# Kernel optimization log

Measured on AMD Instinct MI355X. Metric: run time of the kernel, lower is better.

The kernel has to match this reference:

```python
import jax, jax.numpy as jnp
import numpy as np
import math

B, T, P, E, H = 4, 64, 256, 512, 8
D = E // H
LN_EPS = 1e-5


def setup_inputs() -> dict:
    key = jax.random.key(0)
    ks = jax.random.split(key, 6)
    s = 0.02  # weight init scale
    return {
        "x": jax.random.normal(ks[0], (B, T, P, E), jnp.float32),
        "Wq": jax.random.normal(ks[1], (E, E), jnp.float32) * s,
        "bq": jnp.zeros((E,), jnp.float32),
        "Wk": jax.random.normal(ks[2], (E, E), jnp.float32) * s,
        "bk": jnp.zeros((E,), jnp.float32),
        "Wv": jax.random.normal(ks[3], (E, E), jnp.float32) * s,
        "bv": jnp.zeros((E,), jnp.float32),
        "Wo": jax.random.normal(ks[4], (E, E), jnp.float32) * s,
        "bo": jnp.zeros((E,), jnp.float32),
        "ln_g": jnp.ones((E,), jnp.float32),
        "ln_b": jnp.zeros((E,), jnp.float32),
    }


def _proj(x, W, b):
    # torch nn.Linear: y = x @ W.T + b
    return jnp.einsum('btpe,fe->btpf', x, W) + b


def _heads(y):
    # b t p (h d) -> b p h t d
    b, t, p, e = y.shape
    return y.reshape(b, t, p, H, D).transpose(0, 2, 3, 1, 4)


def reference(x, Wq, bq, Wk, bk, Wv, bv, Wo, bo, ln_g, ln_b):
    b, t, p, e = x.shape
    q = _heads(_proj(x, Wq, bq))  # [B,P,H,T,D]
    k = _heads(_proj(x, Wk, bk))
    v = _heads(_proj(x, Wv, bv))

    scores = jnp.einsum('bphtd,bphsd->bphts', q, k) / math.sqrt(D)
    causal_mask = jnp.triu(jnp.ones((t, t), dtype=bool), k=1)  # True above diag
    scores = jnp.where(causal_mask, -jnp.inf, scores)
    attn = jax.nn.softmax(scores, axis=-1)
    o = jnp.einsum('bphts,bphsd->bphtd', attn, v)

    # b p h t d -> b t p (h d)
    o = o.transpose(0, 3, 1, 2, 4).reshape(b, t, p, e)
    attn_out = jnp.einsum('btpe,fe->btpf', o, Wo) + bo

    y = x + attn_out
    # AdaptiveNormalizer with conditioning=None -> plain LayerNorm over E
    mu = jnp.mean(y, axis=-1, keepdims=True)
    var = jnp.var(y, axis=-1, keepdims=True)
    return (y - mu) * jax.lax.rsqrt(var + LN_EPS) * ln_g + ln_b
```

## Files before the change

### kernel.cpp

```cpp
#include <hip/hip_runtime.h>
#include <stdint.h>

#define B_ 4
#define T_ 64
#define P_ 256
#define E_ 512
#define H_ 8
#define D_ 64
#define NF 1536
#define MCH 16384

typedef unsigned short u16;
typedef __attribute__((ext_vector_type(8))) __bf16 bf16x8;
typedef __attribute__((ext_vector_type(4))) float f32x4;
typedef __attribute__((ext_vector_type(16))) float f32x16;

__device__ __forceinline__ u16 f2bf(float x) {
  union { float f; uint32_t u; } a; a.f = x;
  uint32_t u = a.u;
  uint32_t r = (u + 0x7FFFu + ((u >> 16) & 1u)) >> 16;
  return (u16)r;
}

__device__ __forceinline__ bf16x8 ld8(const u16* p) {
  union { uint4 u; bf16x8 b; } t;
  t.u = *reinterpret_cast<const uint4*>(p);
  return t.b;
}

typedef __attribute__((address_space(3))) void lds_void;
typedef __attribute__((address_space(1))) void g_void;
__device__ __forceinline__ void gl_lds16(const void* g, void* l) {
  __builtin_amdgcn_global_load_lds((g_void*)g, (lds_void*)l, 16, 0, 0);
}

__device__ __forceinline__ f32x4 mfma16(bf16x8 a, bf16x8 b, f32x4 c) {
  return __builtin_amdgcn_mfma_f32_16x16x32_bf16(a, b, c, 0, 0, 0);
}
__device__ __forceinline__ f32x16 mfma32(bf16x8 a, bf16x8 b, f32x16 c) {
  return __builtin_amdgcn_mfma_f32_32x32x16_bf16(a, b, c, 0, 0, 0);
}

#define SBAR() __builtin_amdgcn_s_barrier()

__global__ void cvt_all(const float* __restrict__ x,
                        const float* __restrict__ Wq, const float* __restrict__ Wk,
                        const float* __restrict__ Wv, const float* __restrict__ Wo,
                        u16* __restrict__ xbf, u16* __restrict__ wqkv,
                        u16* __restrict__ wobf) {
  const int idx = blockIdx.x * blockDim.x + threadIdx.x;
  const float* s;
  uint4* d;
  if (idx < 4194304) {
    s = x + (size_t)idx * 8;
    d = reinterpret_cast<uint4*>(xbf) + idx;
  } else {
    const int k = idx - 4194304;
    const int w = k >> 15, off = k & 32767;
    s = ((w == 0) ? Wq : (w == 1) ? Wk : (w == 2) ? Wv : Wo) + (size_t)off * 8;
    d = (w < 3) ? reinterpret_cast<uint4*>(wqkv) + w * 32768 + off
                : reinterpret_cast<uint4*>(wobf) + off;
  }
  const float4* sp = reinterpret_cast<const float4*>(s);
  float4 a = sp[0], b = sp[1];
  union { u16 u[8]; uint4 v; } t;
  t.u[0] = f2bf(a.x); t.u[1] = f2bf(a.y); t.u[2] = f2bf(a.z); t.u[3] = f2bf(a.w);
  t.u[4] = f2bf(b.x); t.u[5] = f2bf(b.y); t.u[6] = f2bf(b.z); t.u[7] = f2bf(b.w);
  *d = t.v;
}

__global__ void cvt_bf16(const float* __restrict__ src, u16* __restrict__ dst, int n8) {
  int i = blockIdx.x * blockDim.x + threadIdx.x;
  if (i >= n8) return;
  const float4* s = reinterpret_cast<const float4*>(src) + (size_t)i * 2;
  float4 a = s[0], b = s[1];
  union { u16 u[8]; uint4 v; } t;
  t.u[0] = f2bf(a.x); t.u[1] = f2bf(a.y); t.u[2] = f2bf(a.z); t.u[3] = f2bf(a.w);
  t.u[4] = f2bf(b.x); t.u[5] = f2bf(b.y); t.u[6] = f2bf(b.z); t.u[7] = f2bf(b.w);
  reinterpret_cast<uint4*>(dst)[i] = t.v;
}
__global__ void cvt_w(const float* __restrict__ Wq, const float* __restrict__ Wk,
                      const float* __restrict__ Wv, const float* __restrict__ Wo,
                      u16* __restrict__ wqkv, u16* __restrict__ wobf) {
  int idx = blockIdx.x * blockDim.x + threadIdx.x;
  int w = idx >> 15;
  int off = idx & 32767;
  const float* s = (w == 0) ? Wq : (w == 1) ? Wk : (w == 2) ? Wv : Wo;
  const float4* sp = reinterpret_cast<const float4*>(s) + (size_t)off * 2;
  float4 a = sp[0], b = sp[1];
  union { u16 u[8]; uint4 v; } t;
  t.u[0] = f2bf(a.x); t.u[1] = f2bf(a.y); t.u[2] = f2bf(a.z); t.u[3] = f2bf(a.w);
  t.u[4] = f2bf(b.x); t.u[5] = f2bf(b.y); t.u[6] = f2bf(b.z); t.u[7] = f2bf(b.w);
  if (w < 3) reinterpret_cast<uint4*>(wqkv)[w * 32768 + off] = t.v;
  else       reinterpret_cast<uint4*>(wobf)[off] = t.v;
}

#define GQ_READA4(E, HH)                                                    \
  _Pragma("unroll") for (int i = 0; i < 4; i++)                             \
  _Pragma("unroll") for (int q = 0; q < 2; q++)                             \
    af[i][q] = ld8(ldsA + ((E) * 2 + (HH)) * 8192 +                         \
                   (wr * 128 + i * 32 + l31) * 32 +                         \
                   ((q * 2 + lhi) ^ xkey) * 8);

#define GQ_READB(E, HH)                                                     \
  _Pragma("unroll") for (int j = 0; j < 2; j++)                             \
  _Pragma("unroll") for (int q = 0; q < 2; q++)                             \
    bfv[j][q] = ld8(ldsB + ((E) * 2 + (HH)) * 8192 +                        \
                    (wc * 64 + j * 32 + l31) * 32 +                         \
                    ((q * 2 + lhi) ^ xkey) * 8);

#define GQ_MFMA16()                                                         \
  __builtin_amdgcn_s_setprio(1);                                            \
  _Pragma("unroll") for (int i = 0; i < 4; i++)                             \
  _Pragma("unroll") for (int j = 0; j < 2; j++)                             \
  _Pragma("unroll") for (int q = 0; q < 2; q++)                             \
    acc[i][j] = mfma32(af[i][q], bfv[j][q], acc[i][j]);                     \
  __builtin_amdgcn_s_setprio(0);

#define GQ_KLOOP()                                                          \
  stageA(0, 0, 0); stageB(0, 0, 0);                                         \
  stageA(0, 1, 0); stageB(0, 1, 0);                                         \
  stageA(1, 0, 1); stageB(1, 0, 1);                                         \
  asm volatile("s_waitcnt vmcnt(8)" ::: "memory");                          \
  SBAR();                                                                   \
  _Pragma("unroll 2") for (int s = 0; s < 8; ++s) {                         \
    const int e = s & 1;                                                    \
    bf16x8 af[4][2], bfv[2][2];                                             \
                                                   \
    GQ_READA4(e, 0)                                                         \
    GQ_READB(e, 0)                                                          \
    if (s < 7) { stageA(e ^ 1, 1, s + 1); stageB(e ^ 1, 1, s + 1);          \
                 asm volatile("s_waitcnt vmcnt(8)" ::: "memory"); }         \
    else       { asm volatile("s_waitcnt vmcnt(0)" ::: "memory"); }         \
    SBAR();                                                                 \
    GQ_MFMA16()                                                             \
    SBAR();                                                                 \
                                                   \
    GQ_READA4(e, 1)                                                         \
    GQ_READB(e, 1)                                                          \
    if (s < 6)      { stageA(e, 0, s + 2); stageB(e, 0, s + 2);             \
                      asm volatile("s_waitcnt vmcnt(8)" ::: "memory"); }    \
    else if (s == 6){ asm volatile("s_waitcnt vmcnt(4)" ::: "memory"); }    \
    SBAR();                                                                 \
    GQ_MFMA16()                                                             \
    SBAR();                                                                 \
  }

__global__ __launch_bounds__(512, 2) void k1_qkv(
    const u16* __restrict__ xbf,
    const u16* __restrict__ wqkv,
    const float* __restrict__ bq, const float* __restrict__ bk, const float* __restrict__ bv,
    u16* __restrict__ qkv)
{
  __shared__ u16 lds[65536];
  u16* ldsA = lds;
  u16* ldsB = lds + 32768;

  const int tid = threadIdx.x;
  const int lane = tid & 63, wid = tid >> 6;
  const int wr = wid >> 2, wc = wid & 3;
  const int l31 = lane & 31, lhi = lane >> 5;
  const int xkey = (l31 >> 1) & 3;

  const int cpx = gridDim.x >> 3;
  const int logical = (blockIdx.x & 7) * cpx + (blockIdx.x >> 3);
  const int m0 = (logical / 6) * 256;
  const int n0 = (logical % 6) * 256;

  const u16* ga = xbf + (size_t)m0 * E_;
  const u16* gb = wqkv + (size_t)n0 * E_;

  const int r0 = tid >> 2;
  const int c0 = ((tid & 3) ^ ((tid >> 3) & 3)) * 8;

  auto stageA = [&](int e, int h, int kt) {
    const int kc = kt * 64 + h * 32;
    u16* base = ldsA + (e * 2 + h) * 8192;
    gl_lds16(ga + (size_t)r0 * E_ + kc + c0, base + wid * 512);
    gl_lds16(ga + (size_t)(r0 + 128) * E_ + kc + c0, base + 4096 + wid * 512);
  };
  auto stageB = [&](int e, int h, int kt) {
    const int kc = kt * 64 + h * 32;
    u16* base = ldsB + (e * 2 + h) * 8192;
    gl_lds16(gb + (size_t)r0 * E_ + kc + c0, base + wid * 512);
    gl_lds16(gb + (size_t)(r0 + 128) * E_ + kc + c0, base + 4096 + wid * 512);
  };

  f32x16 acc[4][2];
#pragma unroll
  for (int i = 0; i < 4; i++)
#pragma unroll
    for (int j = 0; j < 2; j++)
#pragma unroll
      for (int r = 0; r < 16; r++) acc[i][j][r] = 0.f;

  GQ_KLOOP()

  float bias2[2];
#pragma unroll
  for (int j = 0; j < 2; j++) {
    const int fcol = n0 + wc * 64 + j * 32 + l31;
    bias2[j] = fcol < 512 ? bq[fcol] : (fcol < 1024 ? bk[fcol - 512] : bv[fcol - 1024]);
  }
  const int fbase = n0 + wc * 64 + l31;
#pragma unroll
  for (int mi = 0; mi < 4; mi++)
#pragma unroll
    for (int r = 0; r < 16; r++) {
      const size_t row = m0 + wr * 128 + mi * 32 + (r & 3) + 8 * (r >> 2) + 4 * lhi;
      u16* dst = qkv + row * NF + fbase;
      dst[0]  = f2bf(acc[mi][0][r] + bias2[0]);
      dst[32] = f2bf(acc[mi][1][r] + bias2[1]);
    }
}

__global__ __launch_bounds__(256) void k2_attn(
    const u16* __restrict__ qkv,
    u16* __restrict__ o)
{
  __shared__ u16 Pl[4][64 * 72];
  const int tid = threadIdx.x, lane = tid & 63, wid = tid >> 6;
  const int gw = blockIdx.x * 4 + wid;
  const int b = gw >> 11;
  const int g = gw & 2047;
  const int h = g & 7, p = g >> 3;
  const int g4 = lane >> 4;
  const size_t ts = (size_t)P_ * NF;
  const u16* qb = qkv + (size_t)b * MCH * NF + (size_t)p * NF + h * D_;
  const u16* kb = qb + 512;
  const u16* vb = qb + 1024;
  u16* ob = o + (size_t)b * MCH * E_;

  bf16x8 qf[4][2], kf[4][2];
#pragma unroll
  for (int i = 0; i < 4; i++)
#pragma unroll
    for (int ks = 0; ks < 2; ks++) {
      const int rr = i * 16 + (lane & 15);
      const int dc = ks * 32 + g4 * 8;
      qf[i][ks] = ld8(qb + (size_t)rr * ts + dc);
      kf[i][ks] = ld8(kb + (size_t)rr * ts + dc);
    }

  bf16x8 vfr[2][4];
#pragma unroll
  for (int ks = 0; ks < 2; ks++)
#pragma unroll
    for (int ni = 0; ni < 4; ni++) {
      union { u16 u[8]; bf16x8 b; } tv;
#pragma unroll
      for (int j = 0; j < 8; j++) {
        const int s = ks * 32 + g4 * 8 + j;
        tv.u[j] = vb[(size_t)s * ts + ni * 16 + (lane & 15)];
      }
      vfr[ks][ni] = tv.b;
    }

  f32x4 S[4][4];
#pragma unroll
  for (int i = 0; i < 4; i++)
#pragma unroll
    for (int j = 0; j < 4; j++) { f32x4 z = {0.f, 0.f, 0.f, 0.f}; S[i][j] = z; }
#pragma unroll
  for (int ks = 0; ks < 2; ks++)
#pragma unroll
    for (int mi = 0; mi < 4; mi++)
#pragma unroll
      for (int ni = 0; ni < 4; ni++)
        if (ni <= mi)
          S[mi][ni] = mfma16(qf[mi][ks], kf[ni][ks], S[mi][ni]);

  u16* pw = &Pl[wid][0];
#pragma unroll
  for (int mi = 0; mi < 4; mi++)
#pragma unroll
    for (int r = 0; r < 4; r++) {
      const int t = mi * 16 + g4 * 4 + r;
      float v[4]; float mx = -1e30f;
#pragma unroll
      for (int ni = 0; ni < 4; ni++) {
        const int s = ni * 16 + (lane & 15);
        v[ni] = (s <= t) ? S[mi][ni][r] * 0.125f : -1e30f;
        mx = fmaxf(mx, v[ni]);
      }
      mx = fmaxf(mx, __shfl_xor(mx, 1));
      mx = fmaxf(mx, __shfl_xor(mx, 2));
      mx = fmaxf(mx, __shfl_xor(mx, 4));
      mx = fmaxf(mx, __shfl_xor(mx, 8));
      float sum = 0.f; float pv[4];
#pragma unroll
      for (int ni = 0; ni < 4; ni++) {
        const int s = ni * 16 + (lane & 15);
        pv[ni] = (s <= t) ? __expf(v[ni] - mx) : 0.f;
        sum += pv[ni];
      }
      sum += __shfl_xor(sum, 1);
      sum += __shfl_xor(sum, 2);
      sum += __shfl_xor(sum, 4);
      sum += __shfl_xor(sum, 8);
      const float inv = 1.0f / sum;
#pragma unroll
      for (int ni = 0; ni < 4; ni++) {
        const int s = ni * 16 + (lane & 15);
        pw[t * 72 + s] = f2bf(pv[ni] * inv);
      }
    }
  asm volatile("s_waitcnt lgkmcnt(0)" ::: "memory");

  f32x4 O[4][4];
#pragma unroll
  for (int i = 0; i < 4; i++)
#pragma unroll
    for (int j = 0; j < 4; j++) { f32x4 z = {0.f, 0.f, 0.f, 0.f}; O[i][j] = z; }
#pragma unroll
  for (int ks = 0; ks < 2; ks++) {
    bf16x8 pa[4];
#pragma unroll
    for (int mi = 0; mi < 4; mi++)
      pa[mi] = ld8(pw + (mi * 16 + (lane & 15)) * 72 + ks * 32 + g4 * 8);
#pragma unroll
    for (int mi = 0; mi < 4; mi++)
#pragma unroll
      for (int ni = 0; ni < 4; ni++)
        if (!(ks == 1 && mi < 2))
          O[mi][ni] = mfma16(pa[mi], vfr[ks][ni], O[mi][ni]);
  }
#pragma unroll
  for (int mi = 0; mi < 4; mi++)
#pragma unroll
    for (int ni = 0; ni < 4; ni++)
#pragma unroll
      for (int r = 0; r < 4; r++) {
        const int t = mi * 16 + g4 * 4 + r;
        const int d = ni * 16 + (lane & 15);
        ob[((size_t)t * P_ + p) * E_ + h * D_ + d] = f2bf(O[mi][ni][r]);
      }
}

__global__ __launch_bounds__(512, 2) void k3_gemm(
    const u16* __restrict__ obf,
    const u16* __restrict__ wo,
    const float* __restrict__ bo,
    const float* __restrict__ x,
    u16* __restrict__ yb)
{
  __shared__ u16 lds[65536];
  u16* ldsA = lds;
  u16* ldsB = lds + 32768;

  const int tid = threadIdx.x;
  const int lane = tid & 63, wid = tid >> 6;
  const int wr = wid >> 2, wc = wid & 3;
  const int l31 = lane & 31, lhi = lane >> 5;
  const int xkey = (l31 >> 1) & 3;

  const int cpx = gridDim.x >> 3;
  const int logical = (blockIdx.x & 7) * cpx + (blockIdx.x >> 3);
  const int m0 = (logical >> 1) * 256;
  const int n0 = (logical & 1) * 256;

  const u16* ga = obf + (size_t)m0 * E_;
  const u16* gb = wo + (size_t)n0 * E_;

  const int r0 = tid >> 2;
  const int c0 = ((tid & 3) ^ ((tid >> 3) & 3)) * 8;

  auto stageA = [&](int e, int h, int kt) {
    const int kc = kt * 64 + h * 32;
    u16* base = ldsA + (e * 2 + h) * 8192;
    gl_lds16(ga + (size_t)r0 * E_ + kc + c0, base + wid * 512);
    gl_lds16(ga + (size_t)(r0 + 128) * E_ + kc + c0, base + 4096 + wid * 512);
  };
  auto stageB = [&](int e, int h, int kt) {
    const int kc = kt * 64 + h * 32;
    u16* base = ldsB + (e * 2 + h) * 8192;
    gl_lds16(gb + (size_t)r0 * E_ + kc + c0, base + wid * 512);
    gl_lds16(gb + (size_t)(r0 + 128) * E_ + kc + c0, base + 4096 + wid * 512);
  };

  f32x16 acc[4][2];
#pragma unroll
  for (int i = 0; i < 4; i++)
#pragma unroll
    for (int j = 0; j < 2; j++)
#pragma unroll
      for (int r = 0; r < 16; r++) acc[i][j][r] = 0.f;

  GQ_KLOOP()

  float bias2[2];
#pragma unroll
  for (int j = 0; j < 2; j++)
    bias2[j] = bo[n0 + wc * 64 + j * 32 + l31];
  const int fbase = n0 + wc * 64 + l31;
#pragma unroll
  for (int mi = 0; mi < 4; mi++)
#pragma unroll
    for (int r = 0; r < 16; r++) {
      const size_t row = m0 + wr * 128 + mi * 32 + (r & 3) + 8 * (r >> 2) + 4 * lhi;
      u16* dst = yb + row * E_ + fbase;
      const float* xr = x + row * E_ + fbase;
      dst[0]  = f2bf(acc[mi][0][r] + bias2[0] + xr[0]);
      dst[32] = f2bf(acc[mi][1][r] + bias2[1] + xr[32]);
    }
}

__global__ __launch_bounds__(256) void k3_ln(
    const u16* __restrict__ yb, const float* __restrict__ lng,
    const float* __restrict__ lnb, float* __restrict__ out)
{
  const int lane = threadIdx.x & 63;
  const size_t row = (size_t)blockIdx.x * 4 + (threadIdx.x >> 6);
  const int c = lane * 8;
  const uint4 d = *reinterpret_cast<const uint4*>(yb + row * E_ + c);
  const uint32_t* dw = reinterpret_cast<const uint32_t*>(&d);
  float f[8];
#pragma unroll
  for (int j = 0; j < 4; j++) {
    union { uint32_t u; float v; } lo, hi;
    lo.u = dw[j] << 16; hi.u = dw[j] & 0xffff0000u;
    f[2 * j] = lo.v; f[2 * j + 1] = hi.v;
  }
  float s = 0.f, q = 0.f;
#pragma unroll
  for (int j = 0; j < 8; j++) { s += f[j]; q += f[j] * f[j]; }
#pragma unroll
  for (int d2 = 1; d2 < 64; d2 <<= 1) { s += __shfl_xor(s, d2); q += __shfl_xor(q, d2); }
  const float mean = s * (1.0f / 512.0f);
  const float var = q * (1.0f / 512.0f) - mean * mean;
  const float rs = rsqrtf(var + 1e-5f);
  float o8[8];
#pragma unroll
  for (int j = 0; j < 8; j++)
    o8[j] = (f[j] - mean) * rs * lng[c + j] + lnb[c + j];
  float4* op = reinterpret_cast<float4*>(out + row * E_ + c);
  op[0] = make_float4(o8[0], o8[1], o8[2], o8[3]);
  op[1] = make_float4(o8[4], o8[5], o8[6], o8[7]);
}

extern "C" void kernel_launch(void* const* d_in, const int* in_sizes, int n_in,
                              void* d_out, int out_size, void* d_ws, size_t ws_size,
                              hipStream_t stream) {
  const float* x   = (const float*)d_in[0];
  const float* Wq  = (const float*)d_in[1];
  const float* bq  = (const float*)d_in[2];
  const float* Wk  = (const float*)d_in[3];
  const float* bk  = (const float*)d_in[4];
  const float* Wv  = (const float*)d_in[5];
  const float* bv  = (const float*)d_in[6];
  const float* Wo  = (const float*)d_in[7];
  const float* bo  = (const float*)d_in[8];
  const float* lng = (const float*)d_in[9];
  const float* lnb = (const float*)d_in[10];
  float* out = (float*)d_out;
  uint8_t* ws = (uint8_t*)d_ws;

  const size_t NEED_BIG = 270532608ULL;
  if (ws_size >= NEED_BIG) {
    u16* wqkv = (u16*)(ws);
    u16* wobf = (u16*)(ws + 1572864);
    u16* xbf  = (u16*)(ws + 2097152);
    u16* qkvc = (u16*)(ws + 69206016);
    u16* obf  = xbf;
    u16* yb   = qkvc;

    cvt_all<<<16896, 256, 0, stream>>>(x, Wq, Wk, Wv, Wo, xbf, wqkv, wobf);
    k1_qkv<<<1536, 512, 0, stream>>>(xbf, wqkv, bq, bk, bv, qkvc);
    k2_attn<<<2048, 256, 0, stream>>>(qkvc, obf);
    k3_gemm<<<512, 512, 0, stream>>>(obf, wobf, bo, x, yb);
    k3_ln<<<16384, 256, 0, stream>>>(yb, lng, lnb, out);
  } else {
    u16* xbf  = (u16*)(ws);
    u16* qkvc = (u16*)(ws + 16777216);
    u16* obf  = (u16*)(ws + 67108864);
    u16* wqkv = (u16*)(ws + 83886080);
    u16* wobf = (u16*)(ws + 85458944);
    u16* yb   = qkvc;

    cvt_w<<<512, 256, 0, stream>>>(Wq, Wk, Wv, Wo, wqkv, wobf);
    for (int b = 0; b < B_; ++b) {
      const float* xb = x + (size_t)b * MCH * E_;
      cvt_bf16<<<4096, 256, 0, stream>>>(xb, xbf, MCH * E_ / 8);
      k1_qkv<<<384, 512, 0, stream>>>(xbf, wqkv, bq, bk, bv, qkvc);
      k2_attn<<<512, 256, 0, stream>>>(qkvc, obf);
      k3_gemm<<<128, 512, 0, stream>>>(obf, wobf, bo, xb, yb);
      k3_ln<<<4096, 256, 0, stream>>>(yb, lng, lnb, out + (size_t)b * MCH * E_);
    }
  }
}
```

Before: 360.0 us.

## Double-buffer LDS fragment registers to overlap reads with MFMA in QKV GEMM

```diff
diff --git a/kernel.cpp b/kernel.cpp
--- a/kernel.cpp
+++ b/kernel.cpp
@@ -41,7 +41,7 @@
   return __builtin_amdgcn_mfma_f32_32x32x16_bf16(a, b, c, 0, 0, 0);
 }
 
-#define SBAR() __builtin_amdgcn_s_barrier()
+#define SBARF() asm volatile("s_barrier" ::: "memory")
 
 __global__ void cvt_all(const float* __restrict__ x,
                         const float* __restrict__ Wq, const float* __restrict__ Wk,
@@ -95,26 +95,26 @@
   else       reinterpret_cast<uint4*>(wobf)[off] = t.v;
 }
 
-#define GQ_READA4(E, HH)                                                    \
+#define GQ_READA4_TO(AF, E, HH)                                             \
   _Pragma("unroll") for (int i = 0; i < 4; i++)                             \
   _Pragma("unroll") for (int q = 0; q < 2; q++)                             \
-    af[i][q] = ld8(ldsA + ((E) * 2 + (HH)) * 8192 +                         \
+    AF[i][q] = ld8(ldsA + ((E) * 2 + (HH)) * 8192 +                         \
                    (wr * 128 + i * 32 + l31) * 32 +                         \
                    ((q * 2 + lhi) ^ xkey) * 8);
 
-#define GQ_READB(E, HH)                                                     \
+#define GQ_READB_TO(BF, E, HH)                                              \
   _Pragma("unroll") for (int j = 0; j < 2; j++)                             \
   _Pragma("unroll") for (int q = 0; q < 2; q++)                             \
-    bfv[j][q] = ld8(ldsB + ((E) * 2 + (HH)) * 8192 +                        \
-                    (wc * 64 + j * 32 + l31) * 32 +                         \
-                    ((q * 2 + lhi) ^ xkey) * 8);
-
-#define GQ_MFMA16()                                                         \
+    BF[j][q] = ld8(ldsB + ((E) * 2 + (HH)) * 8192 +                         \
+                   (wc * 64 + j * 32 + l31) * 32 +                          \
+                   ((q * 2 + lhi) ^ xkey) * 8);
+
+#define GQ_MFMA_SET(AF, BF)                                                 \
   __builtin_amdgcn_s_setprio(1);                                            \
   _Pragma("unroll") for (int i = 0; i < 4; i++)                             \
   _Pragma("unroll") for (int j = 0; j < 2; j++)                             \
   _Pragma("unroll") for (int q = 0; q < 2; q++)                             \
-    acc[i][j] = mfma32(af[i][q], bfv[j][q], acc[i][j]);                     \
+    acc[i][j] = mfma32(AF[i][q], BF[j][q], acc[i][j]);                      \
   __builtin_amdgcn_s_setprio(0);
 
 #define GQ_KLOOP()                                                          \
@@ -122,28 +122,32 @@
   stageA(0, 1, 0); stageB(0, 1, 0);                                         \
   stageA(1, 0, 1); stageB(1, 0, 1);                                         \
   asm volatile("s_waitcnt vmcnt(8)" ::: "memory");                          \
-  SBAR();                                                                   \
+  SBARF();                                                                  \
+  bf16x8 afA[4][2], bfA[2][2], afB[4][2], bfB[2][2];                        \
+  GQ_READA4_TO(afA, 0, 0)                                                   \
+  GQ_READB_TO(bfA, 0, 0)                                                    \
   _Pragma("unroll 2") for (int s = 0; s < 8; ++s) {                         \
     const int e = s & 1;                                                    \
-    bf16x8 af[4][2], bfv[2][2];                                             \
-                                                   \
-    GQ_READA4(e, 0)                                                         \
-    GQ_READB(e, 0)                                                          \
+        \
     if (s < 7) { stageA(e ^ 1, 1, s + 1); stageB(e ^ 1, 1, s + 1);          \
                  asm volatile("s_waitcnt vmcnt(8)" ::: "memory"); }         \
     else       { asm volatile("s_waitcnt vmcnt(0)" ::: "memory"); }         \
-    SBAR();                                                                 \
-    GQ_MFMA16()                                                             \
-    SBAR();                                                                 \
-                                                   \
-    GQ_READA4(e, 1)                                                         \
-    GQ_READB(e, 1)                                                          \
+    SBARF();                                                                \
+    GQ_READA4_TO(afB, e, 1)                                                 \
+    GQ_READB_TO(bfB, e, 1)                                                  \
+    GQ_MFMA_SET(afA, bfA)                                                   \
+    SBARF();                                                                \
+      \
     if (s < 6)      { stageA(e, 0, s + 2); stageB(e, 0, s + 2);             \
                       asm volatile("s_waitcnt vmcnt(8)" ::: "memory"); }    \
     else if (s == 6){ asm volatile("s_waitcnt vmcnt(4)" ::: "memory"); }    \
-    SBAR();                                                                 \
-    GQ_MFMA16()                                                             \
-    SBAR();                                                                 \
+    SBARF();                                                                \
+    if (s < 7) {                                                            \
+      GQ_READA4_TO(afA, e ^ 1, 0)                                           \
+      GQ_READB_TO(bfA, e ^ 1, 0)                                            \
+    }                                                                       \
+    GQ_MFMA_SET(afB, bfB)                                                   \
+    SBARF();                                                                \
   }
 
 __global__ __launch_bounds__(512, 2) void k1_qkv(
```

New measurement: 378.8 us. +5.2%, slower.
